# Optimization experiments

Hardware: AMD Instinct MI355X
Metric: run time of the kernel (lower is better)

The kernel has to match this reference:

```python
import jax, jax.numpy as jnp
import numpy as np

F = 128          # input feature dim
OUT = 128        # out_channel
MAX_DEG = 10
DEG_COUNTS = np.array([25000, 50000, 100000, 150000, 100000, 50000,
                       5000, 5000, 5000, 5000, 5000], dtype=np.int64)  # deg 0..10
OFFSETS = np.concatenate([[0], np.cumsum(DEG_COUNTS)])  # static bucket offsets
N = int(OFFSETS[-1])  # 500000 atoms


def setup_inputs() -> dict:
    key = jax.random.key(0)
    ks = jax.random.split(key, 16)
    inp = {
        "atom_features": jax.random.normal(ks[0], (N, F), dtype=jnp.float32),
        "deg_slice": jnp.stack([jnp.asarray(OFFSETS[:-1]), jnp.asarray(DEG_COUNTS)],
                               axis=1).astype(jnp.int32),
    }
    for d in range(1, MAX_DEG + 1):
        inp[f"adj{d}"] = jax.random.randint(ks[d], (int(DEG_COUNTS[d]), d), 0, N,
                                            dtype=jnp.int32)
    s = 1.0 / np.sqrt(F)
    inp["W0"] = jax.random.normal(ks[11], (F, OUT), dtype=jnp.float32) * s
    inp["b0"] = jnp.zeros((OUT,), dtype=jnp.float32)
    inp["W_rel"] = jax.random.normal(ks[12], (MAX_DEG, F, OUT), dtype=jnp.float32) * s
    inp["b_rel"] = jnp.zeros((MAX_DEG, OUT), dtype=jnp.float32)
    inp["W_self"] = jax.random.normal(ks[13], (MAX_DEG, F, OUT), dtype=jnp.float32) * s
    inp["b_self"] = jnp.zeros((MAX_DEG, OUT), dtype=jnp.float32)
    return inp


def reference(atom_features, deg_slice, adj1, adj2, adj3, adj4, adj5,
              adj6, adj7, adj8, adj9, adj10,
              W0, b0, W_rel, b_rel, W_self, b_self):
    adjs = (adj1, adj2, adj3, adj4, adj5, adj6, adj7, adj8, adj9, adj10)
    outs = [None] * (MAX_DEG + 1)
    # degree-0 atoms: self transform only (uses the last weight in W_list)
    self0 = atom_features[int(OFFSETS[0]):int(OFFSETS[1])]
    outs[0] = self0 @ W0 + b0
    for d in range(1, MAX_DEG + 1):
        # gather neighbor features: [n_d, d, F], mean over the d neighbors
        rel = jnp.mean(atom_features[adjs[d - 1]], axis=1)
        self_a = atom_features[int(OFFSETS[d]):int(OFFSETS[d + 1])]
        outs[d] = (rel @ W_rel[d - 1] + b_rel[d - 1]
                   + self_a @ W_self[d - 1] + b_self[d - 1])
    return jax.nn.relu(jnp.concatenate(outs, axis=0))
```

## Files before the change

### kernel.cpp

```cpp
#include <hip/hip_runtime.h>

typedef float f32x4 __attribute__((ext_vector_type(4)));
typedef __bf16 bf16x8 __attribute__((ext_vector_type(8)));

#define XS_STRIDE 264

struct AdjPtrs { const int* p[10]; };

__global__ void gc_prep(const float* __restrict__ W0, const float* __restrict__ b0,
                        const float* __restrict__ Wrel, const float* __restrict__ brel,
                        const float* __restrict__ Wself, const float* __restrict__ bself,
                        __bf16* __restrict__ wfrag, float* __restrict__ biasall)
{
    const int id = blockIdx.x * 256 + threadIdx.x;
    {
        const int j    = id & 7;
        const int lane = (id >> 3) & 63;
        const int nt   = (id >> 9) & 7;
        const int ks   = (id >> 12) & 7;
        const int d    = id >> 15;
        const int k = ks * 32 + (lane >> 4) * 8 + j;
        const int n = nt * 16 + (lane & 15);
        float v;
        if (d == 0)      v = (k < 128) ? 0.0f : W0[(k - 128) * 128 + n];
        else if (k < 128) v = Wrel[((d - 1) * 128 + k) * 128 + n];
        else              v = Wself[((d - 1) * 128 + (k - 128)) * 128 + n];
        wfrag[id] = (__bf16)v;
    }
    if (id < 11 * 128) {
        const int dd = id >> 7, c = id & 127;
        biasall[id] = (dd == 0) ? b0[c] : (brel[(dd - 1) * 128 + c] + bself[(dd - 1) * 128 + c]);
    }
}

__global__ __launch_bounds__(256, 4) void gc_main(
    const float* __restrict__ atom, AdjPtrs adj,
    const __bf16* __restrict__ wfrag, const float* __restrict__ biasall,
    float* __restrict__ out)
{
    __shared__ __bf16 Xs[64 * XS_STRIDE];

    const int bid = blockIdx.x;
    int d, tb, off, cnt;
    if      (bid < 391)  { d = 0;  tb = 0;    off = 0;      cnt = 25000;  }
    else if (bid < 1173) { d = 1;  tb = 391;  off = 25000;  cnt = 50000;  }
    else if (bid < 2736) { d = 2;  tb = 1173; off = 75000;  cnt = 100000; }
    else if (bid < 5080) { d = 3;  tb = 2736; off = 175000; cnt = 150000; }
    else if (bid < 6643) { d = 4;  tb = 5080; off = 325000; cnt = 100000; }
    else if (bid < 7425) { d = 5;  tb = 6643; off = 425000; cnt = 50000;  }
    else if (bid < 7504) { d = 6;  tb = 7425; off = 475000; cnt = 5000;   }
    else if (bid < 7583) { d = 7;  tb = 7504; off = 480000; cnt = 5000;   }
    else if (bid < 7662) { d = 8;  tb = 7583; off = 485000; cnt = 5000;   }
    else if (bid < 7741) { d = 9;  tb = 7662; off = 490000; cnt = 5000;   }
    else                 { d = 10; tb = 7741; off = 495000; cnt = 5000;   }
    const int tile = bid - tb;
    const int t = threadIdx.x;

    {
        const int r  = t >> 2;
        const int q  = t & 3;
        const int cb = q * 32;
        const int lr = tile * 64 + r;
        const bool valid = lr < cnt;
        float buf[32];

        #pragma unroll
        for (int i = 0; i < 32; i++) buf[i] = 0.0f;
        if (d > 0 && valid) {
            const int* arow = adj.p[d - 1] + (size_t)lr * d;
            for (int e = 0; e < d; e++) {
                const f32x4* src = (const f32x4*)(atom + (size_t)arow[e] * 128 + cb);
                #pragma unroll
                for (int i = 0; i < 8; i++) {
                    f32x4 v = src[i];
                    buf[4*i+0] += v.x; buf[4*i+1] += v.y;
                    buf[4*i+2] += v.z; buf[4*i+3] += v.w;
                }
            }
            const float sc = 1.0f / (float)d;
            #pragma unroll
            for (int i = 0; i < 32; i++) buf[i] *= sc;
        }
        __bf16* xrow = Xs + r * XS_STRIDE + cb;
        #pragma unroll
        for (int v8 = 0; v8 < 4; v8++) {
            bf16x8 pk;
            #pragma unroll
            for (int j = 0; j < 8; j++) pk[j] = (__bf16)buf[8 * v8 + j];
            *(bf16x8*)(xrow + 8 * v8) = pk;
        }

        #pragma unroll
        for (int i = 0; i < 32; i++) buf[i] = 0.0f;
        if (valid) {
            const f32x4* src = (const f32x4*)(atom + (size_t)(off + lr) * 128 + cb);
            #pragma unroll
            for (int i = 0; i < 8; i++) {
                f32x4 v = src[i];
                buf[4*i+0] = v.x; buf[4*i+1] = v.y;
                buf[4*i+2] = v.z; buf[4*i+3] = v.w;
            }
        }
        xrow = Xs + r * XS_STRIDE + 128 + cb;
        #pragma unroll
        for (int v8 = 0; v8 < 4; v8++) {
            bf16x8 pk;
            #pragma unroll
            for (int j = 0; j < 8; j++) pk[j] = (__bf16)buf[8 * v8 + j];
            *(bf16x8*)(xrow + 8 * v8) = pk;
        }
    }
    __syncthreads();

    const int wave = t >> 6, lane = t & 63;
    const int m16  = lane & 15, quad = lane >> 4;
    const int mbase = (wave & 1) * 32;
    const int ntb   = (wave >> 1) * 4;

    f32x4 acc[2][4];
    {
        f32x4 z; z.x = 0.0f; z.y = 0.0f; z.z = 0.0f; z.w = 0.0f;
        #pragma unroll
        for (int mi = 0; mi < 2; mi++)
            #pragma unroll
            for (int ni = 0; ni < 4; ni++) acc[mi][ni] = z;
    }

    const bf16x8* wbase = (const bf16x8*)wfrag + (size_t)d * 64 * 64 + lane;
    #pragma unroll
    for (int ks = 0; ks < 8; ks++) {
        const bf16x8 a0 = *(const bf16x8*)(Xs + (mbase + m16) * XS_STRIDE + ks * 32 + quad * 8);
        const bf16x8 a1 = *(const bf16x8*)(Xs + (mbase + 16 + m16) * XS_STRIDE + ks * 32 + quad * 8);
        #pragma unroll
        for (int ni = 0; ni < 4; ni++) {
            bf16x8 b = wbase[(size_t)(ks * 8 + ntb + ni) * 64];
            acc[0][ni] = __builtin_amdgcn_mfma_f32_16x16x32_bf16(a0, b, acc[0][ni], 0, 0, 0);
            acc[1][ni] = __builtin_amdgcn_mfma_f32_16x16x32_bf16(a1, b, acc[1][ni], 0, 0, 0);
        }
    }

    #pragma unroll
    for (int ni = 0; ni < 4; ni++) {
        const int col = (ntb + ni) * 16 + m16;
        const float bv = biasall[d * 128 + col];
        #pragma unroll
        for (int mi = 0; mi < 2; mi++) {
            #pragma unroll
            for (int rg = 0; rg < 4; rg++) {
                const int lrow = tile * 64 + mbase + mi * 16 + quad * 4 + rg;
                if (lrow < cnt) {
                    float v = acc[mi][ni][rg] + bv;
                    out[(size_t)(off + lrow) * 128 + col] = fmaxf(v, 0.0f);
                }
            }
        }
    }
}

extern "C" void kernel_launch(void* const* d_in, const int* in_sizes, int n_in,
                              void* d_out, int out_size, void* d_ws, size_t ws_size,
                              hipStream_t stream) {
    const float* atom = (const float*)d_in[0];
    AdjPtrs adj;
    for (int i = 0; i < 10; i++) adj.p[i] = (const int*)d_in[2 + i];
    const float* W0    = (const float*)d_in[12];
    const float* b0    = (const float*)d_in[13];
    const float* Wrel  = (const float*)d_in[14];
    const float* brel  = (const float*)d_in[15];
    const float* Wself = (const float*)d_in[16];
    const float* bself = (const float*)d_in[17];

    __bf16* wfrag   = (__bf16*)d_ws;
    float*  biasall = (float*)((char*)d_ws + 720896);

    hipLaunchKernelGGL(gc_prep, dim3(1408), dim3(256), 0, stream,
                       W0, b0, Wrel, brel, Wself, bself, wfrag, biasall);
    hipLaunchKernelGGL(gc_main, dim3(7820), dim3(256), 0, stream,
                       atom, adj, wfrag, biasall, (float*)d_out);
}
```

Before: 658.9 us.

## Load self features directly into MFMA registers and swizzle the relation tile in LDS

The self-feature half of the A operand is no longer staged through shared memory; each wave reads its rows straight from global memory into registers, converts them to bf16 and feeds the MFMAs, prefetching one k-slice ahead. LDS now holds only the neighbor-mean half with an XOR swizzle instead of padding, which halves shared memory and allows occupancy to rise to 6 blocks per SM. The neighbor gather is templated on degree so index loads and the loop unroll completely, degree-0 blocks skip staging and the barrier, and output uses nontemporal stores. Self rows are now read redundantly by the two wave pairs sharing an M range, and the global loads are less coalesced than the earlier staging path.

```diff
diff --git a/kernel.cpp b/kernel.cpp
--- a/kernel.cpp
+++ b/kernel.cpp
@@ -2,8 +2,7 @@
 
 typedef float f32x4 __attribute__((ext_vector_type(4)));
 typedef __bf16 bf16x8 __attribute__((ext_vector_type(8)));
-
-#define XS_STRIDE 264
+typedef __bf16 bf16x4 __attribute__((ext_vector_type(4)));
 
 struct AdjPtrs { const int* p[10]; };
 
@@ -33,12 +32,64 @@
     }
 }
 
-__global__ __launch_bounds__(256, 4) void gc_main(
+__device__ __forceinline__ int lds_off(int row, int byteoff) {
+    const int chunk = byteoff >> 4;
+    return row * 256 + ((chunk ^ (row & 7)) << 4) + (byteoff & 15);
+}
+
+template<int D>
+__device__ __forceinline__ void stage_rel(const int* __restrict__ adjd,
+                                          const float* __restrict__ atom,
+                                          char* __restrict__ XsB,
+                                          int tile, int cnt, int t)
+{
+    const int r = t >> 2;
+    const int q = t & 3;
+    const int lr = tile * 64 + r;
+
+    float buf[32];
+    #pragma unroll
+    for (int i = 0; i < 32; i++) buf[i] = 0.0f;
+
+    if (lr < cnt) {
+        const int* arow = adjd + (size_t)lr * D;
+        int idx[D];
+        #pragma unroll
+        for (int e = 0; e < D; e++) idx[e] = arow[e];
+        #pragma unroll
+        for (int e = 0; e < D; e++) {
+            const f32x4* src = (const f32x4*)(atom + (size_t)idx[e] * 128) + q;
+            #pragma unroll
+            for (int i = 0; i < 8; i++) {
+                const f32x4 v = src[4 * i];
+                buf[4*i+0] += v[0]; buf[4*i+1] += v[1];
+                buf[4*i+2] += v[2]; buf[4*i+3] += v[3];
+            }
+        }
+        if (D > 1) {
+            constexpr float sc = 1.0f / (float)D;
+            #pragma unroll
+            for (int i = 0; i < 32; i++) buf[i] *= sc;
+        }
+    }
+
+    #pragma unroll
+    for (int i = 0; i < 8; i++) {
+        const int g = q + 4 * i;
+        bf16x4 pk;
+        pk[0] = (__bf16)buf[4*i+0]; pk[1] = (__bf16)buf[4*i+1];
+        pk[2] = (__bf16)buf[4*i+2]; pk[3] = (__bf16)buf[4*i+3];
+        *(bf16x4*)(XsB + lds_off(r, g * 8)) = pk;
+    }
+}
+
+__global__ __launch_bounds__(256, 6) void gc_main(
     const float* __restrict__ atom, AdjPtrs adj,
     const __bf16* __restrict__ wfrag, const float* __restrict__ biasall,
     float* __restrict__ out)
 {
-    __shared__ __bf16 Xs[64 * XS_STRIDE];
+    __shared__ __bf16 Xs[64 * 128];
+    char* XsB = (char*)Xs;
 
     const int bid = blockIdx.x;
     int d, tb, off, cnt;
@@ -56,70 +107,30 @@
     const int tile = bid - tb;
     const int t = threadIdx.x;
 
-    {
-        const int r  = t >> 2;
-        const int q  = t & 3;
-        const int cb = q * 32;
-        const int lr = tile * 64 + r;
-        const bool valid = lr < cnt;
-        float buf[32];
-
-        #pragma unroll
-        for (int i = 0; i < 32; i++) buf[i] = 0.0f;
-        if (d > 0 && valid) {
-            const int* arow = adj.p[d - 1] + (size_t)lr * d;
-            for (int e = 0; e < d; e++) {
-                const f32x4* src = (const f32x4*)(atom + (size_t)arow[e] * 128 + cb);
-                #pragma unroll
-                for (int i = 0; i < 8; i++) {
-                    f32x4 v = src[i];
-                    buf[4*i+0] += v.x; buf[4*i+1] += v.y;
-                    buf[4*i+2] += v.z; buf[4*i+3] += v.w;
-                }
-            }
-            const float sc = 1.0f / (float)d;
-            #pragma unroll
-            for (int i = 0; i < 32; i++) buf[i] *= sc;
-        }
-        __bf16* xrow = Xs + r * XS_STRIDE + cb;
-        #pragma unroll
-        for (int v8 = 0; v8 < 4; v8++) {
-            bf16x8 pk;
-            #pragma unroll
-            for (int j = 0; j < 8; j++) pk[j] = (__bf16)buf[8 * v8 + j];
-            *(bf16x8*)(xrow + 8 * v8) = pk;
-        }
-
-        #pragma unroll
-        for (int i = 0; i < 32; i++) buf[i] = 0.0f;
-        if (valid) {
-            const f32x4* src = (const f32x4*)(atom + (size_t)(off + lr) * 128 + cb);
-            #pragma unroll
-            for (int i = 0; i < 8; i++) {
-                f32x4 v = src[i];
-                buf[4*i+0] = v.x; buf[4*i+1] = v.y;
-                buf[4*i+2] = v.z; buf[4*i+3] = v.w;
-            }
-        }
-        xrow = Xs + r * XS_STRIDE + 128 + cb;
-        #pragma unroll
-        for (int v8 = 0; v8 < 4; v8++) {
-            bf16x8 pk;
-            #pragma unroll
-            for (int j = 0; j < 8; j++) pk[j] = (__bf16)buf[8 * v8 + j];
-            *(bf16x8*)(xrow + 8 * v8) = pk;
-        }
-    }
-    __syncthreads();
-
-    const int wave = t >> 6, lane = t & 63;
+    if (d > 0) {
+        switch (d) {
+            case 1:  stage_rel<1> (adj.p[0], atom, XsB, tile, cnt, t); break;
+            case 2:  stage_rel<2> (adj.p[1], atom, XsB, tile, cnt, t); break;
+            case 3:  stage_rel<3> (adj.p[2], atom, XsB, tile, cnt, t); break;
+            case 4:  stage_rel<4> (adj.p[3], atom, XsB, tile, cnt, t); break;
+            case 5:  stage_rel<5> (adj.p[4], atom, XsB, tile, cnt, t); break;
+            case 6:  stage_rel<6> (adj.p[5], atom, XsB, tile, cnt, t); break;
+            case 7:  stage_rel<7> (adj.p[6], atom, XsB, tile, cnt, t); break;
+            case 8:  stage_rel<8> (adj.p[7], atom, XsB, tile, cnt, t); break;
+            case 9:  stage_rel<9> (adj.p[8], atom, XsB, tile, cnt, t); break;
+            case 10: stage_rel<10>(adj.p[9], atom, XsB, tile, cnt, t); break;
+        }
+        __syncthreads();
+    }
+
+    const int lane = t & 63, wave = t >> 6;
     const int m16  = lane & 15, quad = lane >> 4;
     const int mbase = (wave & 1) * 32;
     const int ntb   = (wave >> 1) * 4;
 
     f32x4 acc[2][4];
     {
-        f32x4 z; z.x = 0.0f; z.y = 0.0f; z.z = 0.0f; z.w = 0.0f;
+        f32x4 z; z[0] = 0.0f; z[1] = 0.0f; z[2] = 0.0f; z[3] = 0.0f;
         #pragma unroll
         for (int mi = 0; mi < 2; mi++)
             #pragma unroll
@@ -127,13 +138,50 @@
     }
 
     const bf16x8* wbase = (const bf16x8*)wfrag + (size_t)d * 64 * 64 + lane;
-    #pragma unroll
-    for (int ks = 0; ks < 8; ks++) {
-        const bf16x8 a0 = *(const bf16x8*)(Xs + (mbase + m16) * XS_STRIDE + ks * 32 + quad * 8);
-        const bf16x8 a1 = *(const bf16x8*)(Xs + (mbase + 16 + m16) * XS_STRIDE + ks * 32 + quad * 8);
+
+    const int lr0 = tile * 64 + mbase + m16;
+    const int lr1 = lr0 + 16;
+    const float* srow0 = atom + (size_t)(off + (lr0 < cnt ? lr0 : cnt - 1)) * 128;
+    const float* srow1 = atom + (size_t)(off + (lr1 < cnt ? lr1 : cnt - 1)) * 128;
+    const int kq = quad * 8;
+
+    f32x4 v00 = ((const f32x4*)(srow0 + kq))[0];
+    f32x4 v01 = ((const f32x4*)(srow0 + kq))[1];
+    f32x4 v10 = ((const f32x4*)(srow1 + kq))[0];
+    f32x4 v11 = ((const f32x4*)(srow1 + kq))[1];
+
+    if (d > 0) {
+        #pragma unroll
+        for (int ks = 0; ks < 4; ks++) {
+            const bf16x8 a0 = *(const bf16x8*)(XsB + lds_off(mbase + m16,      ks * 64 + quad * 16));
+            const bf16x8 a1 = *(const bf16x8*)(XsB + lds_off(mbase + 16 + m16, ks * 64 + quad * 16));
+            #pragma unroll
+            for (int ni = 0; ni < 4; ni++) {
+                const bf16x8 b = wbase[(size_t)(ks * 8 + ntb + ni) * 64];
+                acc[0][ni] = __builtin_amdgcn_mfma_f32_16x16x32_bf16(a0, b, acc[0][ni], 0, 0, 0);
+                acc[1][ni] = __builtin_amdgcn_mfma_f32_16x16x32_bf16(a1, b, acc[1][ni], 0, 0, 0);
+            }
+        }
+    }
+
+    #pragma unroll
+    for (int ksp = 0; ksp < 4; ksp++) {
+        bf16x8 a0, a1;
+        #pragma unroll
+        for (int j = 0; j < 4; j++) {
+            a0[j] = (__bf16)v00[j]; a0[4+j] = (__bf16)v01[j];
+            a1[j] = (__bf16)v10[j]; a1[4+j] = (__bf16)v11[j];
+        }
+        if (ksp < 3) {
+            const int k0 = (ksp + 1) * 32 + kq;
+            v00 = ((const f32x4*)(srow0 + k0))[0];
+            v01 = ((const f32x4*)(srow0 + k0))[1];
+            v10 = ((const f32x4*)(srow1 + k0))[0];
+            v11 = ((const f32x4*)(srow1 + k0))[1];
+        }
         #pragma unroll
         for (int ni = 0; ni < 4; ni++) {
-            bf16x8 b = wbase[(size_t)(ks * 8 + ntb + ni) * 64];
+            const bf16x8 b = wbase[(size_t)((ksp + 4) * 8 + ntb + ni) * 64];
             acc[0][ni] = __builtin_amdgcn_mfma_f32_16x16x32_bf16(a0, b, acc[0][ni], 0, 0, 0);
             acc[1][ni] = __builtin_amdgcn_mfma_f32_16x16x32_bf16(a1, b, acc[1][ni], 0, 0, 0);
         }
@@ -149,8 +197,8 @@
             for (int rg = 0; rg < 4; rg++) {
                 const int lrow = tile * 64 + mbase + mi * 16 + quad * 4 + rg;
                 if (lrow < cnt) {
-                    float v = acc[mi][ni][rg] + bv;
-                    out[(size_t)(off + lrow) * 128 + col] = fmaxf(v, 0.0f);
+                    const float v = fmaxf(acc[mi][ni][rg] + bv, 0.0f);
+                    __builtin_nontemporal_store(v, out + (size_t)(off + lrow) * 128 + col);
                 }
             }
         }
```

Measured after the change: 661.6 us. Within noise of the previous version (+0.4%).
